# Kernel optimization log

Hardware: AMD Instinct MI355X
Metric: run time of the kernel (lower is better)

The kernel has to match this reference:

```python
import jax, jax.numpy as jnp
import numpy as np

H, B, D = 8, 64, 512
EPS = 1e-08


def setup_inputs() -> dict:
    key = jax.random.key(0)
    ks = jax.random.split(key, 4)
    x = jax.random.normal(ks[0], (B, D), dtype=jnp.float32)
    Wq = jax.random.uniform(ks[1], (H, D), dtype=jnp.float32)
    Wk = jax.random.uniform(ks[2], (H, D), dtype=jnp.float32)
    Wv = jax.random.uniform(ks[3], (H, D), dtype=jnp.float32)
    z = jnp.zeros((H, D), dtype=jnp.float32)
    return {"x": x, "Wq": Wq, "bq": z, "Wk": Wk, "bk": z, "Wv": Wv, "bv": z}


def reference(x, Wq, bq, Wk, bk, Wv, bv):
    # per-head elementwise affine: [H,1,D] * [B,D] + [H,1,D] -> [H,B,D]
    q = Wq[:, None, :] * x + bq[:, None, :]
    k = Wk[:, None, :] * x + bk[:, None, :]
    v = Wv[:, None, :] * x + bv[:, None, :]
    # diff[h,b,i,j] = |q[h,b,j] - k[h,b,i]|  (torch: x.unsqueeze(1) - y.unsqueeze(2))
    diff = jnp.abs(q[:, :, None, :] - k[:, :, :, None]) + EPS  # [H,B,D,D]
    sim = jax.nn.softmax(1.0 / diff, axis=-1) / jnp.sqrt(jnp.float32(D))
    # attended[h,b,i] = sum_j sim[h,b,i,j] * v[h,b,j]; then sum over heads
    attended = jnp.einsum('hbij,hbj->bi', sim, v)
    return x + attended
```

## Files before the change

kernel.cpp:

```cpp
#include <hip/hip_runtime.h>
#include <math.h>

#define H 8
#define B 64
#define D 512
#define EPS 1e-8f
#define INV_SQRT_D 0.04419417382415922f
#define LN2 0.6931471805599453f
#define EPS_LN2 6.931471805599453e-9f
#define SCH_A 8388608.0f
#define SCH_B 1064986823.0f

__device__ __forceinline__ float fast_rcp(float x) { return __builtin_amdgcn_rcpf(x); }
__device__ __forceinline__ float fast_exp2(float x) { return __builtin_amdgcn_exp2f(x); }

__device__ __forceinline__ float sch_exp2(float r, float c_row) {
    float u = fmaf(r, SCH_A, c_row);
    u = fmaxf(u, 0.0f);
    return __int_as_float((int)u);
}

__global__ __launch_bounds__(1024, 2) void attn_half(
    const float* __restrict__ x,
    const float* __restrict__ Wq, const float* __restrict__ bq,
    const float* __restrict__ Wk, const float* __restrict__ bk,
    const float* __restrict__ Wv, const float* __restrict__ bv,
    float* __restrict__ ws_att)
{
    const int hb = blockIdx.x;
    const int h = hb >> 6;
    const int b = hb & 63;
    const int t = threadIdx.x;
    const int r = t & (D - 1);
    const int half = t >> 9;

    __shared__ __align__(16) float qs[D];
    __shared__ __align__(16) float vs[D];
    __shared__ float pT[D], pL[D], pA[D];

    const float xv = x[b * D + r];
    const float k = fmaf(Wk[h * D + r], xv, bk[h * D + r]);
    if (half == 0) {
        qs[r] = fmaf(Wq[h * D + r], xv, bq[h * D + r]);
        vs[r] = fmaf(Wv[h * D + r], xv, bv[h * D + r]);
    }
    __syncthreads();

    const float4* q4 = reinterpret_cast<const float4*>(qs) + half * (D / 8);
    const float4* v4 = reinterpret_cast<const float4*>(vs) + half * (D / 8);

    float m0 = INFINITY, m1 = INFINITY, m2 = INFINITY, m3 = INFINITY;
    for (int j = 0; j < D / 8; ++j) {
        const float4 qq = q4[j];
        m0 = fminf(m0, fabsf(qq.x - k));
        m1 = fminf(m1, fabsf(qq.y - k));
        m2 = fminf(m2, fabsf(qq.z - k));
        m3 = fminf(m3, fabsf(qq.w - k));
    }
    const float dmin = fminf(fminf(m0, m1), fminf(m2, m3));
    const float tmax = fast_rcp(fmaf(dmin, LN2, EPS_LN2));
    const float c_row = SCH_B - tmax * SCH_A;

    float l0 = 0.f, l1 = 0.f, l2 = 0.f, l3 = 0.f;
    float a0 = 0.f, a1 = 0.f, a2 = 0.f, a3 = 0.f;
    for (int j = 0; j < D / 8; ++j) {
        const float4 qq = q4[j];
        const float4 vv = v4[j];
        const float r0 = fast_rcp(fmaf(fabsf(qq.x - k), LN2, EPS_LN2));
        const float r1 = fast_rcp(fmaf(fabsf(qq.y - k), LN2, EPS_LN2));
        const float r2 = fast_rcp(fmaf(fabsf(qq.z - k), LN2, EPS_LN2));
        const float r3 = fast_rcp(fmaf(fabsf(qq.w - k), LN2, EPS_LN2));
        const float e0 = sch_exp2(r0, c_row);
        const float e1 = sch_exp2(r1, c_row);
        const float e2 = sch_exp2(r2, c_row);
        const float e3 = sch_exp2(r3, c_row);
        l0 += e0; a0 = fmaf(e0, vv.x, a0);
        l1 += e1; a1 = fmaf(e1, vv.y, a1);
        l2 += e2; a2 = fmaf(e2, vv.z, a2);
        l3 += e3; a3 = fmaf(e3, vv.w, a3);
    }
    const float l = (l0 + l1) + (l2 + l3);
    const float a = (a0 + a1) + (a2 + a3);

    if (half == 1) { pT[r] = tmax; pL[r] = l; pA[r] = a; }
    __syncthreads();
    if (half == 0) {
        const float T1 = pT[r], L1 = pL[r], A1 = pA[r];
        const float m  = fmaxf(tmax, T1);
        const float s0 = fast_exp2(tmax - m);
        const float s1 = fast_exp2(T1 - m);
        const float L  = fmaf(L1, s1, l * s0);
        const float A  = fmaf(A1, s1, a * s0);
        ws_att[hb * D + r] = A * fast_rcp(L) * INV_SQRT_D;
    }
}

__global__ __launch_bounds__(256) void reduce_h(
    const float* __restrict__ x, const float* __restrict__ att,
    float* __restrict__ out)
{
    const int i = blockIdx.x * 256 + threadIdx.x;
    float s = x[i];
    #pragma unroll
    for (int h = 0; h < H; ++h) s += att[h * (B * D) + i];
    out[i] = s;
}

__global__ __launch_bounds__(512) void attn_fused(
    const float* __restrict__ x,
    const float* __restrict__ Wq, const float* __restrict__ bq,
    const float* __restrict__ Wk, const float* __restrict__ bk,
    const float* __restrict__ Wv, const float* __restrict__ bv,
    float* __restrict__ out)
{
    const int b = blockIdx.x;
    const int t = threadIdx.x;

    __shared__ float qs[D];
    __shared__ float vs[D];

    const float xv = x[b * D + t];
    float total = 0.f;

    for (int h = 0; h < H; ++h) {
        __syncthreads();
        qs[t] = Wq[h * D + t] * xv + bq[h * D + t];
        vs[t] = Wv[h * D + t] * xv + bv[h * D + t];
        const float ki = Wk[h * D + t] * xv + bk[h * D + t];
        __syncthreads();

        const float4* q4 = reinterpret_cast<const float4*>(qs);
        const float4* v4 = reinterpret_cast<const float4*>(vs);

        float d0 = INFINITY, d1 = INFINITY, d2 = INFINITY, d3 = INFINITY;
        for (int j = 0; j < D / 4; ++j) {
            float4 qq = q4[j];
            d0 = fminf(d0, fabsf(qq.x - ki));
            d1 = fminf(d1, fabsf(qq.y - ki));
            d2 = fminf(d2, fabsf(qq.z - ki));
            d3 = fminf(d3, fabsf(qq.w - ki));
        }
        const float dmin = fminf(fminf(d0, d1), fminf(d2, d3));
        const float tmax = fast_rcp(fmaf(dmin, LN2, EPS_LN2));

        float l0 = 0.f, l1 = 0.f, l2 = 0.f, l3 = 0.f;
        float a0 = 0.f, a1 = 0.f, a2 = 0.f, a3 = 0.f;
        for (int j = 0; j < D / 4; ++j) {
            float4 qq = q4[j];
            float4 vv = v4[j];
            float e0 = fast_exp2(fast_rcp(fmaf(fabsf(qq.x - ki), LN2, EPS_LN2)) - tmax);
            float e1 = fast_exp2(fast_rcp(fmaf(fabsf(qq.y - ki), LN2, EPS_LN2)) - tmax);
            float e2 = fast_exp2(fast_rcp(fmaf(fabsf(qq.z - ki), LN2, EPS_LN2)) - tmax);
            float e3 = fast_exp2(fast_rcp(fmaf(fabsf(qq.w - ki), LN2, EPS_LN2)) - tmax);
            l0 += e0; a0 = fmaf(e0, vv.x, a0);
            l1 += e1; a1 = fmaf(e1, vv.y, a1);
            l2 += e2; a2 = fmaf(e2, vv.z, a2);
            l3 += e3; a3 = fmaf(e3, vv.w, a3);
        }
        const float l = (l0 + l1) + (l2 + l3);
        const float a = (a0 + a1) + (a2 + a3);
        total += a * fast_rcp(l) * INV_SQRT_D;
    }
    out[b * D + t] = xv + total;
}

extern "C" void kernel_launch(void* const* d_in, const int* in_sizes, int n_in,
                              void* d_out, int out_size, void* d_ws, size_t ws_size,
                              hipStream_t stream) {
    const float* x  = (const float*)d_in[0];
    const float* Wq = (const float*)d_in[1];
    const float* bq = (const float*)d_in[2];
    const float* Wk = (const float*)d_in[3];
    const float* bk = (const float*)d_in[4];
    const float* Wv = (const float*)d_in[5];
    const float* bv = (const float*)d_in[6];
    float* out = (float*)d_out;

    const size_t need = (size_t)H * B * D * sizeof(float);

    if (ws_size >= need) {
        float* ws = (float*)d_ws;
        attn_half<<<H * B, 1024, 0, stream>>>(x, Wq, bq, Wk, bk, Wv, bv, ws);
        reduce_h<<<(B * D) / 256, 256, 0, stream>>>(x, ws, out);
    } else {
        attn_fused<<<B, 512, 0, stream>>>(x, Wq, bq, Wk, bk, Wv, bv, out);
    }
}
```

Before: 36.51 us.

## Fuse head reduction into attention kernel by remapping blocks to batch-row chunks

```diff
diff --git a/kernel.cpp b/kernel.cpp
--- a/kernel.cpp
+++ b/kernel.cpp
@@ -15,39 +15,50 @@
 __device__ __forceinline__ float fast_exp2(float x) { return __builtin_amdgcn_exp2f(x); }
 
 __device__ __forceinline__ float sch_exp2(float r, float c_row) {
-    float u = fmaf(r, SCH_A, c_row);
-    u = fmaxf(u, 0.0f);
-    return __int_as_float((int)u);
+    const float u = fmaf(r, SCH_A, c_row);
+    return __uint_as_float((unsigned)u);
 }
 
-__global__ __launch_bounds__(1024, 2) void attn_half(
+__global__ __launch_bounds__(1024, 2) void attn_all(
     const float* __restrict__ x,
     const float* __restrict__ Wq, const float* __restrict__ bq,
     const float* __restrict__ Wk, const float* __restrict__ bk,
     const float* __restrict__ Wv, const float* __restrict__ bv,
-    float* __restrict__ ws_att)
+    float* __restrict__ out)
 {
-    const int hb = blockIdx.x;
-    const int h = hb >> 6;
-    const int b = hb & 63;
+    const int blk = blockIdx.x;
+    const int b = blk >> 3;
+    const int chunk = blk & 7;
     const int t = threadIdx.x;
-    const int r = t & (D - 1);
+    const int r6 = t & 63;
+    const int h = (t >> 6) & 7;
     const int half = t >> 9;
+    const int i = chunk * 64 + r6;
 
-    __shared__ __align__(16) float qs[D];
-    __shared__ __align__(16) float vs[D];
-    __shared__ float pT[D], pL[D], pA[D];
+    __shared__ __align__(16) float qs[H * D];
+    __shared__ __align__(16) float vs[H * D];
+    __shared__ float mT[H * 64], mL[H * 64], mA[H * 64];
 
-    const float xv = x[b * D + r];
-    const float k = fmaf(Wk[h * D + r], xv, bk[h * D + r]);
-    if (half == 0) {
-        qs[r] = fmaf(Wq[h * D + r], xv, bq[h * D + r]);
-        vs[r] = fmaf(Wv[h * D + r], xv, bv[h * D + r]);
+    {
+        const float4 wq = reinterpret_cast<const float4*>(Wq)[t];
+        const float4 bqv = reinterpret_cast<const float4*>(bq)[t];
+        const float4 wv = reinterpret_cast<const float4*>(Wv)[t];
+        const float4 bvv = reinterpret_cast<const float4*>(bv)[t];
+        const float4 xx = reinterpret_cast<const float4*>(x + b * D)[t & 127];
+        float4 qq, vv;
+        qq.x = fmaf(wq.x, xx.x, bqv.x);  vv.x = fmaf(wv.x, xx.x, bvv.x);
+        qq.y = fmaf(wq.y, xx.y, bqv.y);  vv.y = fmaf(wv.y, xx.y, bvv.y);
+        qq.z = fmaf(wq.z, xx.z, bqv.z);  vv.z = fmaf(wv.z, xx.z, bvv.z);
+        qq.w = fmaf(wq.w, xx.w, bqv.w);  vv.w = fmaf(wv.w, xx.w, bvv.w);
+        reinterpret_cast<float4*>(qs)[t] = qq;
+        reinterpret_cast<float4*>(vs)[t] = vv;
     }
+    const float xi = x[b * D + i];
+    const float k = fmaf(Wk[h * D + i], xi, bk[h * D + i]);
     __syncthreads();
 
-    const float4* q4 = reinterpret_cast<const float4*>(qs) + half * (D / 8);
-    const float4* v4 = reinterpret_cast<const float4*>(vs) + half * (D / 8);
+    const float4* q4 = reinterpret_cast<const float4*>(qs + h * D) + half * (D / 8);
+    const float4* v4 = reinterpret_cast<const float4*>(vs + h * D) + half * (D / 8);
 
     float m0 = INFINITY, m1 = INFINITY, m2 = INFINITY, m3 = INFINITY;
     for (int j = 0; j < D / 8; ++j) {
@@ -82,86 +93,25 @@
     const float l = (l0 + l1) + (l2 + l3);
     const float a = (a0 + a1) + (a2 + a3);
 
-    if (half == 1) { pT[r] = tmax; pL[r] = l; pA[r] = a; }
+    if (half == 1) { mT[h * 64 + r6] = tmax; mL[h * 64 + r6] = l; mA[h * 64 + r6] = a; }
     __syncthreads();
     if (half == 0) {
-        const float T1 = pT[r], L1 = pL[r], A1 = pA[r];
+        const float T1 = mT[h * 64 + r6], L1 = mL[h * 64 + r6], A1 = mA[h * 64 + r6];
         const float m  = fmaxf(tmax, T1);
         const float s0 = fast_exp2(tmax - m);
         const float s1 = fast_exp2(T1 - m);
         const float L  = fmaf(L1, s1, l * s0);
         const float A  = fmaf(A1, s1, a * s0);
-        ws_att[hb * D + r] = A * fast_rcp(L) * INV_SQRT_D;
+        mT[h * 64 + r6] = A * fast_rcp(L) * INV_SQRT_D;
     }
-}
+    __syncthreads();
 
-__global__ __launch_bounds__(256) void reduce_h(
-    const float* __restrict__ x, const float* __restrict__ att,
-    float* __restrict__ out)
-{
-    const int i = blockIdx.x * 256 + threadIdx.x;
-    float s = x[i];
-    #pragma unroll
-    for (int h = 0; h < H; ++h) s += att[h * (B * D) + i];
-    out[i] = s;
-}
-
-__global__ __launch_bounds__(512) void attn_fused(
-    const float* __restrict__ x,
-    const float* __restrict__ Wq, const float* __restrict__ bq,
-    const float* __restrict__ Wk, const float* __restrict__ bk,
-    const float* __restrict__ Wv, const float* __restrict__ bv,
-    float* __restrict__ out)
-{
-    const int b = blockIdx.x;
-    const int t = threadIdx.x;
-
-    __shared__ float qs[D];
-    __shared__ float vs[D];
-
-    const float xv = x[b * D + t];
-    float total = 0.f;
-
-    for (int h = 0; h < H; ++h) {
-        __syncthreads();
-        qs[t] = Wq[h * D + t] * xv + bq[h * D + t];
-        vs[t] = Wv[h * D + t] * xv + bv[h * D + t];
-        const float ki = Wk[h * D + t] * xv + bk[h * D + t];
-        __syncthreads();
-
-        const float4* q4 = reinterpret_cast<const float4*>(qs);
-        const float4* v4 = reinterpret_cast<const float4*>(vs);
-
-        float d0 = INFINITY, d1 = INFINITY, d2 = INFINITY, d3 = INFINITY;
-        for (int j = 0; j < D / 4; ++j) {
-            float4 qq = q4[j];
-            d0 = fminf(d0, fabsf(qq.x - ki));
-            d1 = fminf(d1, fabsf(qq.y - ki));
-            d2 = fminf(d2, fabsf(qq.z - ki));
-            d3 = fminf(d3, fabsf(qq.w - ki));
-        }
-        const float dmin = fminf(fminf(d0, d1), fminf(d2, d3));
-        const float tmax = fast_rcp(fmaf(dmin, LN2, EPS_LN2));
-
-        float l0 = 0.f, l1 = 0.f, l2 = 0.f, l3 = 0.f;
-        float a0 = 0.f, a1 = 0.f, a2 = 0.f, a3 = 0.f;
-        for (int j = 0; j < D / 4; ++j) {
-            float4 qq = q4[j];
-            float4 vv = v4[j];
-            float e0 = fast_exp2(fast_rcp(fmaf(fabsf(qq.x - ki), LN2, EPS_LN2)) - tmax);
-            float e1 = fast_exp2(fast_rcp(fmaf(fabsf(qq.y - ki), LN2, EPS_LN2)) - tmax);
-            float e2 = fast_exp2(fast_rcp(fmaf(fabsf(qq.z - ki), LN2, EPS_LN2)) - tmax);
-            float e3 = fast_exp2(fast_rcp(fmaf(fabsf(qq.w - ki), LN2, EPS_LN2)) - tmax);
-            l0 += e0; a0 = fmaf(e0, vv.x, a0);
-            l1 += e1; a1 = fmaf(e1, vv.y, a1);
-            l2 += e2; a2 = fmaf(e2, vv.z, a2);
-            l3 += e3; a3 = fmaf(e3, vv.w, a3);
-        }
-        const float l = (l0 + l1) + (l2 + l3);
-        const float a = (a0 + a1) + (a2 + a3);
-        total += a * fast_rcp(l) * INV_SQRT_D;
+    if (t < 64) {
+        float s = xi;
+        #pragma unroll
+        for (int hh = 0; hh < H; ++hh) s += mT[hh * 64 + t];
+        out[b * D + chunk * 64 + t] = s;
     }
-    out[b * D + t] = xv + total;
 }
 
 extern "C" void kernel_launch(void* const* d_in, const int* in_sizes, int n_in,
@@ -176,13 +126,5 @@
     const float* bv = (const float*)d_in[6];
     float* out = (float*)d_out;
 
-    const size_t need = (size_t)H * B * D * sizeof(float);
-
-    if (ws_size >= need) {
-        float* ws = (float*)d_ws;
-        attn_half<<<H * B, 1024, 0, stream>>>(x, Wq, bq, Wk, bk, Wv, bv, ws);
-        reduce_h<<<(B * D) / 256, 256, 0, stream>>>(x, ws, out);
-    } else {
-        attn_fused<<<B, 512, 0, stream>>>(x, Wq, bq, Wk, bk, Wv, bv, out);
-    }
+    attn_all<<<B * (D / 64), 1024, 0, stream>>>(x, Wq, bq, Wk, bk, Wv, bv, out);
 }
```

Measured after the change: 31.84 us. -12.8%, faster.
